# Optimization experiments

Hardware: AMD Instinct MI355X
Metric: run time of the kernel (lower is better)

Reference implementation:

```python
import jax, jax.numpy as jnp
import numpy as np

D_MODEL = 1024
N_HEADS = 16
D_HEAD = D_MODEL // N_HEADS


def setup_inputs() -> dict:
    key = jax.random.key(0)
    kx, kq, kk, kv, ko = jax.random.split(key, 5)
    s = 1.0 / np.sqrt(D_MODEL)
    return {
        "x": jax.random.normal(kx, (4, 2048, D_MODEL), dtype=jnp.float32),
        "Wq": jax.random.normal(kq, (D_MODEL, D_MODEL), dtype=jnp.float32) * s,
        "Wk": jax.random.normal(kk, (D_MODEL, D_MODEL), dtype=jnp.float32) * s,
        "Wv": jax.random.normal(kv, (D_MODEL, D_MODEL), dtype=jnp.float32) * s,
        "Wo": jax.random.normal(ko, (D_MODEL, D_MODEL), dtype=jnp.float32) * s,
    }


def reference(x, Wq, Wk, Wv, Wo):
    B, L, D = x.shape
    # Projections (torch Linear: y = x @ W.T)
    q = (x @ Wq.T).reshape(B, L, N_HEADS, D_HEAD).transpose(0, 2, 1, 3)  # [B,H,L,dh]
    k = (x @ Wk.T).reshape(B, L, N_HEADS, D_HEAD).transpose(0, 2, 1, 3)
    v = (x @ Wv.T).reshape(B, L, N_HEADS, D_HEAD).transpose(0, 2, 1, 3)
    scale = 1.0 / np.sqrt(D_HEAD).astype(np.float32)
    scores = jnp.einsum('bhqd,bhkd->bhqk', q, k) * scale  # [B,H,L,L]
    causal = jnp.tril(jnp.ones((L, L), dtype=bool))
    scores = jnp.where(causal[None, None], scores, -jnp.inf)
    attn = jax.nn.softmax(scores, axis=-1)
    out = jnp.einsum('bhqk,bhkd->bhqd', attn, v)  # [B,H,L,dh]
    out = out.transpose(0, 2, 1, 3).reshape(B, L, D)
    return out @ Wo.T
```

## Files before the change

kernel.cpp:

```cpp
#include <hip/hip_runtime.h>

typedef short bf16x8 __attribute__((ext_vector_type(8)));
typedef float f32x4 __attribute__((ext_vector_type(4)));
typedef unsigned short u16;

#define MFMA16x16x32(a, b, c) __builtin_amdgcn_mfma_f32_16x16x32_bf16((a), (b), (c), 0, 0, 0)

#define BATCH 4
#define SEQ 2048
#define DMODEL 1024
#define NHEADS 16
#define DHEAD 64
#define MROWS (BATCH * SEQ)

#define QSCALE 0.18033688011112443f

__device__ __forceinline__ u16 f2bf(float f) {
  unsigned u = __builtin_bit_cast(unsigned, f);
  u += 0x7fffu + ((u >> 16) & 1u);
  return (u16)(u >> 16);
}

__device__ __forceinline__ void gl_lds16(const u16* g, u16* l) {
  __builtin_amdgcn_global_load_lds((__attribute__((address_space(1))) void*)g,
                                   (__attribute__((address_space(3))) void*)l, 16, 0, 0);
}

template <int CTRL>
__device__ __forceinline__ float dppmov(float x) {
  return __builtin_bit_cast(
      float, __builtin_amdgcn_mov_dpp(__builtin_bit_cast(int, x), CTRL, 0xF, 0xF, false));
}
__device__ __forceinline__ float rowmax16(float x) {
  x = fmaxf(x, dppmov<0x128>(x));
  x = fmaxf(x, dppmov<0x124>(x));
  x = fmaxf(x, dppmov<0x122>(x));
  x = fmaxf(x, dppmov<0x121>(x));
  return x;
}
__device__ __forceinline__ float rowsum16(float x) {
  x += dppmov<0x128>(x);
  x += dppmov<0x124>(x);
  x += dppmov<0x122>(x);
  x += dppmov<0x121>(x);
  return x;
}

__global__ void cvt_all(const float* __restrict__ x, const float* __restrict__ wq,
                        const float* __restrict__ wk, const float* __restrict__ wv,
                        const float* __restrict__ wo, u16* __restrict__ xb,
                        u16* __restrict__ wqb, u16* __restrict__ wkb, u16* __restrict__ wvb,
                        u16* __restrict__ wob) {
  int blk = blockIdx.x;
  const float* src;
  u16* dst;
  long off;
  if (blk < 8192) {
    src = x; dst = xb;
    off = (long)blk * 256 + threadIdx.x;
  } else {
    int ws = (blk - 8192) >> 10;
    int wb = (blk - 8192) & 1023;
    src = ws == 0 ? wq : ws == 1 ? wk : ws == 2 ? wv : wo;
    dst = ws == 0 ? wqb : ws == 1 ? wkb : ws == 2 ? wvb : wob;
    off = (long)wb * 256 + threadIdx.x;
  }
  float4 v = reinterpret_cast<const float4*>(src)[off];
  ushort4 o;
  o.x = f2bf(v.x); o.y = f2bf(v.y); o.z = f2bf(v.z); o.w = f2bf(v.w);
  reinterpret_cast<ushort4*>(dst)[off] = o;
}

__device__ __forceinline__ void gemm_core(const u16* __restrict__ A, const u16* __restrict__ Bm,
                                          int row0, int bcol0, u16* As, u16* Bs,
                                          f32x4 (*acc)[4], int tid) {
  const int lane = tid & 63, w = tid >> 6;
  const int wr = w >> 1, wc = w & 1;
  const int quad = lane >> 4, l16 = lane & 15;
  const int lr = lane >> 3;
  const int lcs = ((lane & 7) ^ lr) * 8;
  const int sw = (l16 & 7) * 8;

  const long abase = (long)(row0 + lr) * 1024 + lcs;
  const long bbase = (long)(bcol0 + lr) * 1024 + lcs;

  for (int k0 = 0; k0 < 1024; k0 += 64) {
#pragma unroll
    for (int i = 0; i < 4; i++) {
      int rb = i * 32 + w * 8;
      gl_lds16(&A[abase + (long)rb * 1024 + k0], &As[rb * 64]);
      gl_lds16(&Bm[bbase + (long)rb * 1024 + k0], &Bs[rb * 64]);
    }
    __syncthreads();
#pragma unroll
    for (int ks = 0; ks < 2; ks++) {
      bf16x8 af[4], bfr[4];
#pragma unroll
      for (int i = 0; i < 4; i++)
        af[i] = *reinterpret_cast<const bf16x8*>(
            &As[(wr * 64 + i * 16 + l16) * 64 + (((ks * 32 + quad * 8)) ^ sw)]);
#pragma unroll
      for (int j = 0; j < 4; j++)
        bfr[j] = *reinterpret_cast<const bf16x8*>(
            &Bs[(wc * 64 + j * 16 + l16) * 64 + (((ks * 32 + quad * 8)) ^ sw)]);
#pragma unroll
      for (int i = 0; i < 4; i++)
#pragma unroll
        for (int j = 0; j < 4; j++)
          acc[i][j] = MFMA16x16x32(af[i], bfr[j], acc[i][j]);
    }
    __syncthreads();
  }
}

__global__ __launch_bounds__(256) void gemm_qkv(const u16* __restrict__ xb,
                                                const u16* __restrict__ wqb,
                                                const u16* __restrict__ wkb,
                                                const u16* __restrict__ wvb,
                                                u16* __restrict__ qb, u16* __restrict__ kb,
                                                u16* __restrict__ vtb) {
  __shared__ u16 As[128 * 64];
  __shared__ u16 Bs[128 * 64];
  const int tid = threadIdx.x;
  const int lane = tid & 63, w = tid >> 6;
  const int wr = w >> 1, wc = w & 1;
  const int quad = lane >> 4, l16 = lane & 15;
  const int row0 = blockIdx.y * 128;
  const int col0 = blockIdx.x * 128;
  const int widx = col0 >> 10;
  const int bcol0 = col0 & 1023;
  const u16* Bm = widx == 0 ? wqb : (widx == 1 ? wkb : wvb);

  f32x4 acc[4][4] = {};
  gemm_core(xb, Bm, row0, bcol0, As, Bs, acc, tid);

#pragma unroll
  for (int i = 0; i < 4; i++)
#pragma unroll
    for (int j = 0; j < 4; j++)
#pragma unroll
      for (int r = 0; r < 4; r++) {
        int row = row0 + wr * 64 + i * 16 + quad * 4 + r;
        int col = bcol0 + wc * 64 + j * 16 + l16;
        float v = acc[i][j][r];
        int bh = ((row >> 11) << 4) | (col >> 6);
        if (widx == 0) {
          qb[(bh * SEQ + (row & 2047)) * DHEAD + (col & 63)] = f2bf(v * QSCALE);
        } else if (widx == 1) {
          kb[(bh * SEQ + (row & 2047)) * DHEAD + (col & 63)] = f2bf(v);
        } else {
          vtb[(bh * DHEAD + (col & 63)) * SEQ + (row & 2047)] = f2bf(v);
        }
      }
}

__global__ __launch_bounds__(256) void gemm_out(const u16* __restrict__ aob,
                                                const u16* __restrict__ wob,
                                                float* __restrict__ out) {
  __shared__ u16 As[128 * 64];
  __shared__ u16 Bs[128 * 64];
  const int tid = threadIdx.x;
  const int lane = tid & 63, w = tid >> 6;
  const int wr = w >> 1, wc = w & 1;
  const int quad = lane >> 4, l16 = lane & 15;
  const int row0 = blockIdx.y * 128;
  const int col0 = blockIdx.x * 128;

  f32x4 acc[4][4] = {};
  gemm_core(aob, wob, row0, col0, As, Bs, acc, tid);

#pragma unroll
  for (int i = 0; i < 4; i++)
#pragma unroll
    for (int j = 0; j < 4; j++)
#pragma unroll
      for (int r = 0; r < 4; r++) {
        int row = row0 + wr * 64 + i * 16 + quad * 4 + r;
        int col = col0 + wc * 64 + j * 16 + l16;
        out[(long)row * DMODEL + col] = acc[i][j][r];
      }
}

__global__ __launch_bounds__(256, 3) void attn_kernel(const u16* __restrict__ Q,
                                                      const u16* __restrict__ Kk,
                                                      const u16* __restrict__ Vt,
                                                      u16* __restrict__ Ao) {
  constexpr int STR = 72;
  __shared__ u16 Ks[64 * STR];
  __shared__ u16 Vs[64 * STR];
  __shared__ u16 Plds[4][32 * STR];
  const int tid = threadIdx.x;
  const int lane = tid & 63;
  const int w = tid >> 6;
  const int quad = lane >> 4, l16 = lane & 15;
  const int bh = blockIdx.x & 63;
  const int qt = 15 - (blockIdx.x >> 6);
  const int b = bh >> 4, h = bh & 15;
  const u16* Qh = Q + bh * SEQ * DHEAD;
  const u16* Kh = Kk + bh * SEQ * DHEAD;
  const u16* Vh = Vt + bh * DHEAD * SEQ;
  const int q0w = qt * 128 + w * 32;
  const int nkt = 2 * qt + 2;

  bf16x8 qf[2][2];
#pragma unroll
  for (int rt = 0; rt < 2; rt++)
#pragma unroll
    for (int ks = 0; ks < 2; ks++)
      qf[rt][ks] = *reinterpret_cast<const bf16x8*>(
          &Qh[(q0w + rt * 16 + l16) * DHEAD + ks * 32 + quad * 8]);

  f32x4 o[2][4] = {};
  float m_i[2][4], l_i[2][4];
#pragma unroll
  for (int rt = 0; rt < 2; rt++)
#pragma unroll
    for (int r = 0; r < 4; r++) { m_i[rt][r] = -1e30f; l_i[rt][r] = 0.f; }

  const int srow = tid >> 3;
  const int scol = (tid & 7) * 8;
  bf16x8 kst[2], vst[2];
  auto load_tile = [&](int kb) {
#pragma unroll
    for (int c = 0; c < 2; c++) {
      int r = srow + c * 32;
      kst[c] = *reinterpret_cast<const bf16x8*>(&Kh[(kb + r) * DHEAD + scol]);
      vst[c] = *reinterpret_cast<const bf16x8*>(&Vh[r * SEQ + kb + scol]);
    }
  };
  auto store_tile = [&]() {
#pragma unroll
    for (int c = 0; c < 2; c++) {
      int r = srow + c * 32;
      *reinterpret_cast<bf16x8*>(&Ks[r * STR + scol]) = kst[c];
      *reinterpret_cast<bf16x8*>(&Vs[r * STR + scol]) = vst[c];
    }
  };

  load_tile(0);
  store_tile();
  __syncthreads();

  for (int kt = 0; kt < nkt; kt++) {
    const int kbase = kt * 64;
    const bool have_next = (kt + 1 < nkt);
    if (have_next) load_tile(kbase + 64);

    if (kbase <= q0w + 31) {
      f32x4 s[2][4];
#pragma unroll
      for (int nt = 0; nt < 4; nt++) {
        bf16x8 kf0 = *reinterpret_cast<const bf16x8*>(&Ks[(nt * 16 + l16) * STR + quad * 8]);
        bf16x8 kf1 = *reinterpret_cast<const bf16x8*>(&Ks[(nt * 16 + l16) * STR + 32 + quad * 8]);
#pragma unroll
        for (int rt = 0; rt < 2; rt++) {
          f32x4 z = {0.f, 0.f, 0.f, 0.f};
          z = MFMA16x16x32(qf[rt][0], kf0, z);
          s[rt][nt] = MFMA16x16x32(qf[rt][1], kf1, z);
        }
      }
      if (kbase + 63 > q0w) {
#pragma unroll
        for (int rt = 0; rt < 2; rt++)
#pragma unroll
          for (int nt = 0; nt < 4; nt++)
#pragma unroll
            for (int r = 0; r < 4; r++) {
              int qrow = q0w + rt * 16 + quad * 4 + r;
              int kcol = kbase + nt * 16 + l16;
              if (kcol > qrow) s[rt][nt][r] = -1e30f;
            }
      }
      float alpha[2][4];
#pragma unroll
      for (int rt = 0; rt < 2; rt++)
#pragma unroll
        for (int r = 0; r < 4; r++) {
          float mx = fmaxf(fmaxf(s[rt][0][r], s[rt][1][r]), fmaxf(s[rt][2][r], s[rt][3][r]));
          mx = rowmax16(mx);
          float mnew = fmaxf(m_i[rt][r], mx);
          alpha[rt][r] = exp2f(m_i[rt][r] - mnew);
          m_i[rt][r] = mnew;
        }
#pragma unroll
      for (int rt = 0; rt < 2; rt++)
#pragma unroll
        for (int nt = 0; nt < 4; nt++)
#pragma unroll
          for (int r = 0; r < 4; r++)
            s[rt][nt][r] = exp2f(s[rt][nt][r] - m_i[rt][r]);
#pragma unroll
      for (int rt = 0; rt < 2; rt++)
#pragma unroll
        for (int r = 0; r < 4; r++) {
          float rs = (s[rt][0][r] + s[rt][1][r]) + (s[rt][2][r] + s[rt][3][r]);
          rs = rowsum16(rs);
          l_i[rt][r] = l_i[rt][r] * alpha[rt][r] + rs;
        }
#pragma unroll
      for (int rt = 0; rt < 2; rt++)
#pragma unroll
        for (int nt = 0; nt < 4; nt++)
#pragma unroll
          for (int r = 0; r < 4; r++) o[rt][nt][r] *= alpha[rt][r];
      u16* Pw = Plds[w];
#pragma unroll
      for (int rt = 0; rt < 2; rt++)
#pragma unroll
        for (int nt = 0; nt < 4; nt++)
#pragma unroll
          for (int r = 0; r < 4; r++)
            Pw[(rt * 16 + quad * 4 + r) * STR + nt * 16 + l16] = f2bf(s[rt][nt][r]);
      asm volatile("s_waitcnt lgkmcnt(0)" ::: "memory");
      bf16x8 pa[2][2];
#pragma unroll
      for (int rt = 0; rt < 2; rt++)
#pragma unroll
        for (int hh = 0; hh < 2; hh++)
          pa[rt][hh] = *reinterpret_cast<const bf16x8*>(
              &Pw[(rt * 16 + l16) * STR + hh * 32 + quad * 8]);
#pragma unroll
      for (int nt2 = 0; nt2 < 4; nt2++) {
        bf16x8 vf0 = *reinterpret_cast<const bf16x8*>(&Vs[(nt2 * 16 + l16) * STR + quad * 8]);
        bf16x8 vf1 = *reinterpret_cast<const bf16x8*>(&Vs[(nt2 * 16 + l16) * STR + 32 + quad * 8]);
#pragma unroll
        for (int rt = 0; rt < 2; rt++) {
          o[rt][nt2] = MFMA16x16x32(pa[rt][0], vf0, o[rt][nt2]);
          o[rt][nt2] = MFMA16x16x32(pa[rt][1], vf1, o[rt][nt2]);
        }
      }
    }

    if (have_next) {
      __syncthreads();
      store_tile();
      __syncthreads();
    }
  }

#pragma unroll
  for (int rt = 0; rt < 2; rt++)
#pragma unroll
    for (int nt2 = 0; nt2 < 4; nt2++)
#pragma unroll
      for (int r = 0; r < 4; r++) {
        int qrow = q0w + rt * 16 + quad * 4 + r;
        float v = o[rt][nt2][r] / l_i[rt][r];
        Ao[(b * SEQ + qrow) * DMODEL + h * DHEAD + nt2 * 16 + l16] = f2bf(v);
      }
}

extern "C" void kernel_launch(void* const* d_in, const int* in_sizes, int n_in,
                              void* d_out, int out_size, void* d_ws, size_t ws_size,
                              hipStream_t stream) {
  const float* x = (const float*)d_in[0];
  const float* Wq = (const float*)d_in[1];
  const float* Wk = (const float*)d_in[2];
  const float* Wv = (const float*)d_in[3];
  const float* Wo = (const float*)d_in[4];
  float* out = (float*)d_out;

  u16* xb  = (u16*)d_ws;
  u16* wqb = xb  + MROWS * DMODEL;
  u16* wkb = wqb + DMODEL * DMODEL;
  u16* wvb = wkb + DMODEL * DMODEL;
  u16* wob = wvb + DMODEL * DMODEL;
  u16* qb  = wob + DMODEL * DMODEL;
  u16* kb  = qb  + MROWS * DMODEL;
  u16* vtb = kb  + MROWS * DMODEL;
  u16* aob = vtb + MROWS * DMODEL;

  cvt_all<<<12288, 256, 0, stream>>>(x, Wq, Wk, Wv, Wo, xb, wqb, wkb, wvb, wob);

  gemm_qkv<<<dim3(24, 64), 256, 0, stream>>>(xb, wqb, wkb, wvb, qb, kb, vtb);

  attn_kernel<<<BATCH * NHEADS * (SEQ / 128), 256, 0, stream>>>(qb, kb, vtb, aob);

  gemm_out<<<dim3(8, 64), 256, 0, stream>>>(aob, wob, out);
}
```

Measured before the change: 293.5 us.

## Double-buffer attention K/V tiles via direct global-to-LDS loads with XOR swizzle

The attention kernel now stages K and V tiles into two LDS buffers using global_load_lds, replacing the register round-trip and store. The next tile's load is issued right after a single barrier, so it overlaps with compute on the current buffer. An XOR swizzle replaces row padding to avoid bank conflicts, and exp2f is swapped for the hardware exp2 builtin when available. LDS use grows from the double buffers, which may reduce occupancy at three blocks per CU, and the builtin exp2 gives up exp2f's denormal handling.

```diff
diff --git a/kernel.cpp b/kernel.cpp
--- a/kernel.cpp
+++ b/kernel.cpp
@@ -14,6 +14,15 @@
 #define MROWS (BATCH * SEQ)
 
 #define QSCALE 0.18033688011112443f
+
+#if defined(__has_builtin)
+#if __has_builtin(__builtin_amdgcn_exp2f)
+#define EXP2(x) __builtin_amdgcn_exp2f(x)
+#endif
+#endif
+#ifndef EXP2
+#define EXP2(x) exp2f(x)
+#endif
 
 __device__ __forceinline__ u16 f2bf(float f) {
   unsigned u = __builtin_bit_cast(unsigned, f);
@@ -98,11 +107,11 @@
 #pragma unroll
       for (int i = 0; i < 4; i++)
         af[i] = *reinterpret_cast<const bf16x8*>(
-            &As[(wr * 64 + i * 16 + l16) * 64 + (((ks * 32 + quad * 8)) ^ sw)]);
+            &As[(wr * 64 + i * 16 + l16) * 64 + ((ks * 32 + quad * 8) ^ sw)]);
 #pragma unroll
       for (int j = 0; j < 4; j++)
         bfr[j] = *reinterpret_cast<const bf16x8*>(
-            &Bs[(wc * 64 + j * 16 + l16) * 64 + (((ks * 32 + quad * 8)) ^ sw)]);
+            &Bs[(wc * 64 + j * 16 + l16) * 64 + ((ks * 32 + quad * 8) ^ sw)]);
 #pragma unroll
       for (int i = 0; i < 4; i++)
 #pragma unroll
@@ -185,10 +194,10 @@
                                                       const u16* __restrict__ Kk,
                                                       const u16* __restrict__ Vt,
                                                       u16* __restrict__ Ao) {
-  constexpr int STR = 72;
-  __shared__ u16 Ks[64 * STR];
-  __shared__ u16 Vs[64 * STR];
-  __shared__ u16 Plds[4][32 * STR];
+  constexpr int PSTR = 72;
+  __shared__ u16 Ksb[2][64 * 64];
+  __shared__ u16 Vsb[2][64 * 64];
+  __shared__ u16 Plds[4][32 * PSTR];
   const int tid = threadIdx.x;
   const int lane = tid & 63;
   const int w = tid >> 6;
@@ -202,6 +211,10 @@
   const int q0w = qt * 128 + w * 32;
   const int nkt = 2 * qt + 2;
 
+  const int lr = lane >> 3;
+  const int swcol = ((lane & 7) ^ lr) * 8;
+  const int sw = (l16 & 7) * 8;
+
   bf16x8 qf[2][2];
 #pragma unroll
   for (int rt = 0; rt < 2; rt++)
@@ -217,41 +230,35 @@
 #pragma unroll
     for (int r = 0; r < 4; r++) { m_i[rt][r] = -1e30f; l_i[rt][r] = 0.f; }
 
-  const int srow = tid >> 3;
-  const int scol = (tid & 7) * 8;
-  bf16x8 kst[2], vst[2];
-  auto load_tile = [&](int kb) {
-#pragma unroll
-    for (int c = 0; c < 2; c++) {
-      int r = srow + c * 32;
-      kst[c] = *reinterpret_cast<const bf16x8*>(&Kh[(kb + r) * DHEAD + scol]);
-      vst[c] = *reinterpret_cast<const bf16x8*>(&Vh[r * SEQ + kb + scol]);
+  auto stage = [&](int kb, int bufi) {
+    u16* Kd = Ksb[bufi];
+    u16* Vd = Vsb[bufi];
+#pragma unroll
+    for (int i = 0; i < 2; i++) {
+      int r = w * 16 + i * 8;
+      gl_lds16(&Kh[(long)(kb + r + lr) * DHEAD + swcol], &Kd[r * 64]);
+      gl_lds16(&Vh[(long)(r + lr) * SEQ + kb + swcol], &Vd[r * 64]);
     }
   };
-  auto store_tile = [&]() {
-#pragma unroll
-    for (int c = 0; c < 2; c++) {
-      int r = srow + c * 32;
-      *reinterpret_cast<bf16x8*>(&Ks[r * STR + scol]) = kst[c];
-      *reinterpret_cast<bf16x8*>(&Vs[r * STR + scol]) = vst[c];
-    }
-  };
-
-  load_tile(0);
-  store_tile();
-  __syncthreads();
+
+  stage(0, 0);
 
   for (int kt = 0; kt < nkt; kt++) {
     const int kbase = kt * 64;
-    const bool have_next = (kt + 1 < nkt);
-    if (have_next) load_tile(kbase + 64);
+    asm volatile("s_waitcnt vmcnt(0) lgkmcnt(0)\n\ts_barrier" ::: "memory");
+    if (kt + 1 < nkt) stage(kbase + 64, (kt + 1) & 1);
+
+    const u16* Ks = Ksb[kt & 1];
+    const u16* Vs = Vsb[kt & 1];
 
     if (kbase <= q0w + 31) {
       f32x4 s[2][4];
 #pragma unroll
       for (int nt = 0; nt < 4; nt++) {
-        bf16x8 kf0 = *reinterpret_cast<const bf16x8*>(&Ks[(nt * 16 + l16) * STR + quad * 8]);
-        bf16x8 kf1 = *reinterpret_cast<const bf16x8*>(&Ks[(nt * 16 + l16) * STR + 32 + quad * 8]);
+        bf16x8 kf0 = *reinterpret_cast<const bf16x8*>(
+            &Ks[(nt * 16 + l16) * 64 + ((quad * 8) ^ sw)]);
+        bf16x8 kf1 = *reinterpret_cast<const bf16x8*>(
+            &Ks[(nt * 16 + l16) * 64 + ((32 + quad * 8) ^ sw)]);
 #pragma unroll
         for (int rt = 0; rt < 2; rt++) {
           f32x4 z = {0.f, 0.f, 0.f, 0.f};
@@ -279,7 +286,7 @@
           float mx = fmaxf(fmaxf(s[rt][0][r], s[rt][1][r]), fmaxf(s[rt][2][r], s[rt][3][r]));
           mx = rowmax16(mx);
           float mnew = fmaxf(m_i[rt][r], mx);
-          alpha[rt][r] = exp2f(m_i[rt][r] - mnew);
+          alpha[rt][r] = EXP2(m_i[rt][r] - mnew);
           m_i[rt][r] = mnew;
         }
 #pragma unroll
@@ -288,7 +295,7 @@
         for (int nt = 0; nt < 4; nt++)
 #pragma unroll
           for (int r = 0; r < 4; r++)
-            s[rt][nt][r] = exp2f(s[rt][nt][r] - m_i[rt][r]);
+            s[rt][nt][r] = EXP2(s[rt][nt][r] - m_i[rt][r]);
 #pragma unroll
       for (int rt = 0; rt < 2; rt++)
 #pragma unroll
@@ -310,7 +317,7 @@
         for (int nt = 0; nt < 4; nt++)
 #pragma unroll
           for (int r = 0; r < 4; r++)
-            Pw[(rt * 16 + quad * 4 + r) * STR + nt * 16 + l16] = f2bf(s[rt][nt][r]);
+            Pw[(rt * 16 + quad * 4 + r) * PSTR + nt * 16 + l16] = f2bf(s[rt][nt][r]);
       asm volatile("s_waitcnt lgkmcnt(0)" ::: "memory");
       bf16x8 pa[2][2];
 #pragma unroll
@@ -318,23 +325,19 @@
 #pragma unroll
         for (int hh = 0; hh < 2; hh++)
           pa[rt][hh] = *reinterpret_cast<const bf16x8*>(
-              &Pw[(rt * 16 + l16) * STR + hh * 32 + quad * 8]);
+              &Pw[(rt * 16 + l16) * PSTR + hh * 32 + quad * 8]);
 #pragma unroll
       for (int nt2 = 0; nt2 < 4; nt2++) {
-        bf16x8 vf0 = *reinterpret_cast<const bf16x8*>(&Vs[(nt2 * 16 + l16) * STR + quad * 8]);
-        bf16x8 vf1 = *reinterpret_cast<const bf16x8*>(&Vs[(nt2 * 16 + l16) * STR + 32 + quad * 8]);
+        bf16x8 vf0 = *reinterpret_cast<const bf16x8*>(
+            &Vs[(nt2 * 16 + l16) * 64 + ((quad * 8) ^ sw)]);
+        bf16x8 vf1 = *reinterpret_cast<const bf16x8*>(
+            &Vs[(nt2 * 16 + l16) * 64 + ((32 + quad * 8) ^ sw)]);
 #pragma unroll
         for (int rt = 0; rt < 2; rt++) {
           o[rt][nt2] = MFMA16x16x32(pa[rt][0], vf0, o[rt][nt2]);
           o[rt][nt2] = MFMA16x16x32(pa[rt][1], vf1, o[rt][nt2]);
         }
       }
-    }
-
-    if (have_next) {
-      __syncthreads();
-      store_tile();
-      __syncthreads();
     }
   }
 
```

Result: no change. 290.6 us (-1.0%).
